# Kernel optimization log

Measured on AMD Instinct MI355X. Metric: run time of the kernel, lower is better.

## Reference

```python
import jax, jax.numpy as jnp
import numpy as np

N = 50000   # nodes
E = 640000  # edges
D_IN = 128
D_OUT = 128
EPS = 1e-5


def _layer_norm(x, gamma, beta):
    mu = jnp.mean(x, axis=-1, keepdims=True)
    var = jnp.mean(jnp.square(x - mu), axis=-1, keepdims=True)
    return (x - mu) * jax.lax.rsqrt(var + EPS) * gamma + beta


def _sage_conv(x, src, dst, w_l, b_l, w_r):
    # PyG SAGEConv (aggr='mean', root_weight=True, normalize=False):
    #   out = lin_l(mean_{j in N(i)} x_j) + lin_r(x_i)
    msgs = x[src]                                             # [E, D]
    agg = jax.ops.segment_sum(msgs, dst, num_segments=N)      # [N, D]
    cnt = jax.ops.segment_sum(jnp.ones((E,), x.dtype), dst, num_segments=N)
    mean = agg / jnp.maximum(cnt, 1.0)[:, None]
    return mean @ w_l.T + b_l + x @ w_r.T


def setup_inputs() -> dict:
    key = jax.random.key(0)
    ks = jax.random.split(key, 12)
    s_in = 1.0 / np.sqrt(D_IN)
    s_out = 1.0 / np.sqrt(D_OUT)
    return {
        "x": jax.random.normal(ks[0], (N, D_IN), jnp.float32),
        "edges": jax.random.randint(ks[1], (2, E), 0, N),
        "dp_w": jax.random.uniform(ks[2], (D_OUT, D_IN), jnp.float32, -s_in, s_in),
        "dp_b": jnp.zeros((D_OUT,), jnp.float32),
        "sc_w": jax.random.uniform(ks[3], (D_OUT, D_IN), jnp.float32, -s_in, s_in),
        "sc_b": jnp.zeros((D_OUT,), jnp.float32),
        "g1_lw": jax.random.uniform(ks[4], (D_OUT, D_OUT), jnp.float32, -s_out, s_out),
        "g1_lb": jnp.zeros((D_OUT,), jnp.float32),
        "g1_rw": jax.random.uniform(ks[5], (D_OUT, D_OUT), jnp.float32, -s_out, s_out),
        "n1_g": jnp.ones((D_OUT,), jnp.float32),
        "n1_b": jnp.zeros((D_OUT,), jnp.float32),
        "g2_lw": jax.random.uniform(ks[6], (D_OUT, D_OUT), jnp.float32, -s_out, s_out),
        "g2_lb": jnp.zeros((D_OUT,), jnp.float32),
        "g2_rw": jax.random.uniform(ks[7], (D_OUT, D_OUT), jnp.float32, -s_out, s_out),
        "n2_g": jnp.ones((D_OUT,), jnp.float32),
        "n2_b": jnp.zeros((D_OUT,), jnp.float32),
    }


def reference(x, edges, dp_w, dp_b, sc_w, sc_b, g1_lw, g1_lb, g1_rw, n1_g, n1_b,
              g2_lw, g2_lb, g2_rw, n2_g, n2_b):
    gelu = lambda v: jax.nn.gelu(v, approximate=False)
    src, dst = edges[0], edges[1]
    shortcut = x @ sc_w.T + sc_b
    h = gelu(x @ dp_w.T + dp_b)
    h = _sage_conv(h, src, dst, g1_lw, g1_lb, g1_rw)
    h = gelu(_layer_norm(h, n1_g, n1_b))
    h = _sage_conv(h, src, dst, g2_lw, g2_lb, g2_rw)
    h = _layer_norm(h, n2_g, n2_b)
    return gelu(h + shortcut)
```

## Files before the change

### kernel.cpp

```cpp
#include <hip/hip_runtime.h>
#include <hip/hip_bf16.h>
#include <math.h>

#define D 128
#define WS 136
#define FS 132
#define PB 128

typedef __attribute__((ext_vector_type(8))) short bf16x8;
typedef __attribute__((ext_vector_type(4))) float f32x4;

__device__ __forceinline__ unsigned short f2bf(float f){
  return (unsigned short)((__float_as_uint(f) + 0x8000u) >> 16);
}
__device__ __forceinline__ float bf2f(unsigned short h){
  return __uint_as_float(((unsigned)h) << 16);
}
__device__ __forceinline__ float bf2f_lo(unsigned v){
  return __uint_as_float(v << 16);
}
__device__ __forceinline__ float bf2f_hi(unsigned v){
  return __uint_as_float(v & 0xFFFF0000u);
}
__device__ __forceinline__ float gelu_fast(float v){
  float u = v * v;
  float arg = v * (1.5957691216f + 0.0713548163f * u);
  arg = fminf(arg, 60.0f);
  float e = __expf(arg);
  return v * e * __builtin_amdgcn_rcpf(e + 1.0f);
}

__global__ __launch_bounds__(256) void k_prepcnt(const float* s0, const float* s1,
    const float* s2, const float* s3, const float* s4, const float* s5,
    unsigned short* dst, const int* __restrict__ edst, int* __restrict__ cnt,
    int E, int nbuck, int epb){
  __shared__ int hist[512];
  if (blockIdx.x < 48){
    int gt = blockIdx.x * 256 + threadIdx.x;
    int m = gt >> 11;
    int r = gt & 2047;
    int f = r >> 6, lane = r & 63;
    int t = f & 7, kk = f >> 3;
    int row = t * 16 + (lane & 15);
    int col = kk * 32 + (lane >> 4) * 8;
    const float* src;
    if (m == 0) src = s0; else if (m == 1) src = s1; else if (m == 2) src = s2;
    else if (m == 3) src = s3; else if (m == 4) src = s4; else src = s5;
    src += row * 128 + col;
    float4 a = *(const float4*)src;
    float4 bb = *(const float4*)(src + 4);
    bf16x8 o;
    o[0] = (short)f2bf(a.x);  o[1] = (short)f2bf(a.y);
    o[2] = (short)f2bf(a.z);  o[3] = (short)f2bf(a.w);
    o[4] = (short)f2bf(bb.x); o[5] = (short)f2bf(bb.y);
    o[6] = (short)f2bf(bb.z); o[7] = (short)f2bf(bb.w);
    int pair = m >> 1, half = m & 1;
    *(bf16x8*)(dst + (size_t)pair * 32768 + (((size_t)f * 2 + half) * 64 + lane) * 8) = o;
    return;
  }
  int blk = blockIdx.x - 48;
  for (int b = threadIdx.x; b < nbuck; b += 256) hist[b] = 0;
  __syncthreads();
  int start = blk * epb;
  int end = min(E, start + epb);
  for (int e = start + threadIdx.x; e < end; e += 256)
    atomicAdd(&hist[edst[e] >> 7], 1);
  __syncthreads();
  for (int b = threadIdx.x; b < nbuck; b += 256) cnt[blk * nbuck + b] = hist[b];
}

__global__ __launch_bounds__(128) void k_scanA(const int* __restrict__ cnt,
    int* __restrict__ offs_rel, int* __restrict__ tot, int nbuck){
  __shared__ int sm[128];
  int b = blockIdx.x, t = threadIdx.x;
  int v = cnt[t * nbuck + b];
  sm[t] = v; __syncthreads();
  for (int ofs = 1; ofs < 128; ofs <<= 1){
    int u = (t >= ofs) ? sm[t - ofs] : 0;
    __syncthreads();
    sm[t] += u;
    __syncthreads();
  }
  offs_rel[t * nbuck + b] = sm[t] - v;
  if (t == 127) tot[b] = sm[127];
}

__global__ __launch_bounds__(256) void k_pscatter(const int* __restrict__ esrc,
    const int* __restrict__ edst, const int* __restrict__ offs_rel,
    const int* __restrict__ tot, unsigned* __restrict__ ebuf,
    int E, int nbuck, int epb){
  __shared__ int stot[512];
  __shared__ int loff[512];
  for (int b = threadIdx.x; b < nbuck; b += 256) stot[b] = tot[b];
  __syncthreads();
  for (int b = threadIdx.x; b < nbuck; b += 256){
    int s = 0;
    for (int j = 0; j < b; j++) s += stot[j];
    loff[b] = s + offs_rel[blockIdx.x * nbuck + b];
  }
  __syncthreads();
  int start = blockIdx.x * epb;
  int end = min(E, start + epb);
  for (int e = start + threadIdx.x; e < end; e += 256){
    int s = esrc[e], d = edst[e];
    int b = d >> 7;
    int pos = atomicAdd(&loff[b], 1);
    ebuf[pos] = (unsigned)s | ((unsigned)(d & 127) << 16);
  }
}

__global__ __launch_bounds__(256) void k_csrin(
    const unsigned* __restrict__ ebuf, const int* __restrict__ tot,
    int* __restrict__ off, int* __restrict__ csr,
    const float* __restrict__ x, const unsigned short* __restrict__ wp,
    const float* __restrict__ scb, const float* __restrict__ dpb,
    unsigned short* __restrict__ sbuf, unsigned short* __restrict__ hbuf,
    int N, int E, int nbuck){
  __shared__ int cnt[128], pref[128], curs[128];
  __shared__ int stot[512], red[256];
  __shared__ unsigned short tile[64 * WS];
  int tid = threadIdx.x;
  if ((int)blockIdx.x < nbuck){
    int b = blockIdx.x;
    for (int j = tid; j < nbuck; j += 256) stot[j] = tot[j];
    __syncthreads();
    int part = 0;
    for (int j = tid; j < b; j += 256) part += stot[j];
    red[tid] = part;
    __syncthreads();
    for (int ofs = 128; ofs > 0; ofs >>= 1){
      if (tid < ofs) red[tid] += red[tid + ofs];
      __syncthreads();
    }
    int start = red[0];
    int end = start + stot[b];
    if (tid < 128) cnt[tid] = 0;
    __syncthreads();
    for (int e = start + tid; e < end; e += 256)
      atomicAdd(&cnt[ebuf[e] >> 16], 1);
    __syncthreads();
    if (tid < 128) pref[tid] = cnt[tid];
    __syncthreads();
    for (int ofs = 1; ofs < 128; ofs <<= 1){
      int v = 0;
      if (tid < 128 && tid >= ofs) v = pref[tid - ofs];
      __syncthreads();
      if (tid < 128) pref[tid] += v;
      __syncthreads();
    }
    if (tid < 128){
      int ex = pref[tid] - cnt[tid];
      curs[tid] = ex;
      int node = b * 128 + tid;
      if (node < N) off[node] = start + ex;
    }
    if (b == 0 && tid == 0) off[N] = E;
    __syncthreads();
    for (int e = start + tid; e < end; e += 256){
      unsigned u = ebuf[e];
      int d = u >> 16;
      int p = atomicAdd(&curs[d], 1);
      csr[start + p] = (int)(u & 0xFFFFu);
    }
    return;
  }
  int bx = blockIdx.x - nbuck;
  int w = tid >> 6, lane = tid & 63, quad = lane >> 4, l16 = lane & 15;
  int nbb = bx * 64;
  int nb = nbb + w * 16;
  int arow = min(nb + l16, N - 1);
  f32x4 acc[2][8];
  #pragma unroll
  for (int m = 0; m < 2; m++)
    #pragma unroll
    for (int t = 0; t < 8; t++) acc[m][t] = (f32x4){0.f, 0.f, 0.f, 0.f};
  #pragma unroll
  for (int kk = 0; kk < 4; kk++){
    const float* xp = x + (size_t)arow * D + kk * 32 + quad * 8;
    float4 xa = *(const float4*)xp;
    float4 xb = *(const float4*)(xp + 4);
    bf16x8 a;
    a[0] = (short)f2bf(xa.x); a[1] = (short)f2bf(xa.y);
    a[2] = (short)f2bf(xa.z); a[3] = (short)f2bf(xa.w);
    a[4] = (short)f2bf(xb.x); a[5] = (short)f2bf(xb.y);
    a[6] = (short)f2bf(xb.z); a[7] = (short)f2bf(xb.w);
    #pragma unroll
    for (int t = 0; t < 8; t++){
      size_t fo = (((size_t)(kk * 8 + t) * 2) * 64 + lane) * 8;
      bf16x8 b0 = *(const bf16x8*)(wp + fo);
      bf16x8 b1 = *(const bf16x8*)(wp + fo + 512);
      acc[0][t] = __builtin_amdgcn_mfma_f32_16x16x32_bf16(a, b0, acc[0][t], 0, 0, 0);
      acc[1][t] = __builtin_amdgcn_mfma_f32_16x16x32_bf16(a, b1, acc[1][t], 0, 0, 0);
    }
  }
  #pragma unroll
  for (int m = 0; m < 2; m++){
    const float* bias = m ? dpb : scb;
    #pragma unroll
    for (int t = 0; t < 8; t++){
      float bv = bias[t * 16 + l16];
      #pragma unroll
      for (int r = 0; r < 4; r++){
        int nl = w * 16 + quad * 4 + r;
        float v = acc[m][t][r] + bv;
        if (m) v = gelu_fast(v);
        tile[nl * WS + t * 16 + l16] = f2bf(v);
      }
    }
    __syncthreads();
    unsigned short* dst = m ? hbuf : sbuf;
    #pragma unroll
    for (int i = 0; i < 4; i++){
      int c = tid + 256 * i;
      int nl = c >> 4, j = c & 15;
      int node = nbb + nl;
      if (node < N)
        *(bf16x8*)(dst + (size_t)node * D + j * 8) = *(const bf16x8*)(tile + nl * WS + j * 8);
    }
    __syncthreads();
  }
}

__global__ __launch_bounds__(256) void k_gather(
    const unsigned short* __restrict__ hin,
    const int* __restrict__ off, const int* __restrict__ csr,
    unsigned short* __restrict__ mout, int N){
  int tid = threadIdx.x;
  int node = blockIdx.x * 16 + (tid >> 4);
  int l16 = tid & 15;
  if (node >= N) return;
  int s0 = off[node], s1 = off[node + 1];
  float acc[8];
  #pragma unroll
  for (int c = 0; c < 8; c++) acc[c] = 0.f;
  if (s1 > s0){
    const unsigned short* hp = hin + l16 * 8;
    int nn[8];
    #pragma unroll
    for (int i = 0; i < 8; i++) nn[i] = csr[min(s0 + i, s1 - 1)];
    for (int e = s0; e < s1; e += 8){
      uint4 v[8];
      #pragma unroll
      for (int i = 0; i < 8; i++)
        v[i] = *(const uint4*)(hp + (size_t)nn[i] * D);
      #pragma unroll
      for (int i = 0; i < 8; i++) nn[i] = csr[min(e + 8 + i, s1 - 1)];
      #pragma unroll
      for (int i = 0; i < 8; i++){
        float m = (e + i < s1) ? 1.f : 0.f;
        acc[0] += m * bf2f_lo(v[i].x);
        acc[1] += m * bf2f_hi(v[i].x);
        acc[2] += m * bf2f_lo(v[i].y);
        acc[3] += m * bf2f_hi(v[i].y);
        acc[4] += m * bf2f_lo(v[i].z);
        acc[5] += m * bf2f_hi(v[i].z);
        acc[6] += m * bf2f_lo(v[i].w);
        acc[7] += m * bf2f_hi(v[i].w);
      }
    }
  }
  float inv = 1.f / (float)max(s1 - s0, 1);
  bf16x8 o;
  #pragma unroll
  for (int c = 0; c < 8; c++) o[c] = (short)f2bf(acc[c] * inv);
  *(bf16x8*)(mout + (size_t)node * D + l16 * 8) = o;
}

__global__ __launch_bounds__(256) void k_gemm(
    const unsigned short* __restrict__ hin,
    const unsigned short* __restrict__ mbuf,
    const unsigned short* __restrict__ wp,
    const float* __restrict__ lb, const float* __restrict__ gamma,
    const float* __restrict__ beta,
    const unsigned short* __restrict__ sbuf,
    unsigned short* __restrict__ hout, float* __restrict__ fout, int N, int mode){
  extern __shared__ char smraw[];
  unsigned short* stile = (unsigned short*)smraw;
  float* ftile = (float*)smraw;
  int tid = threadIdx.x;
  int nbb = blockIdx.x * 64;
  int w = tid >> 6, lane = tid & 63, quad = lane >> 4, l16 = lane & 15;
  int nb = nbb + w * 16;
  int arow = min(nb + l16, N - 1);
  bf16x8 am[4], ah[4];
  #pragma unroll
  for (int kk = 0; kk < 4; kk++){
    am[kk] = *(const bf16x8*)(mbuf + (size_t)arow * D + kk * 32 + quad * 8);
    ah[kk] = *(const bf16x8*)(hin + (size_t)arow * D + kk * 32 + quad * 8);
  }
  f32x4 acc[8];
  #pragma unroll
  for (int t = 0; t < 8; t++) acc[t] = (f32x4){0.f, 0.f, 0.f, 0.f};
  #pragma unroll
  for (int kk = 0; kk < 4; kk++){
    #pragma unroll
    for (int t = 0; t < 8; t++){
      size_t fo = (((size_t)(kk * 8 + t) * 2) * 64 + lane) * 8;
      bf16x8 bl = *(const bf16x8*)(wp + fo);
      bf16x8 br = *(const bf16x8*)(wp + fo + 512);
      acc[t] = __builtin_amdgcn_mfma_f32_16x16x32_bf16(am[kk], bl, acc[t], 0, 0, 0);
      acc[t] = __builtin_amdgcn_mfma_f32_16x16x32_bf16(ah[kk], br, acc[t], 0, 0, 0);
    }
  }
  float lbv[8], gv[8], bv[8];
  #pragma unroll
  for (int t = 0; t < 8; t++){
    lbv[t] = lb[t * 16 + l16];
    gv[t] = gamma[t * 16 + l16];
    bv[t] = beta[t * 16 + l16];
  }
  float mu[4], rs[4];
  #pragma unroll
  for (int r = 0; r < 4; r++){
    float s = 0.f, qq = 0.f;
    #pragma unroll
    for (int t = 0; t < 8; t++){
      float v = acc[t][r] + lbv[t];
      acc[t][r] = v;
      s += v; qq += v * v;
    }
    s += __shfl_xor(s, 1); qq += __shfl_xor(qq, 1);
    s += __shfl_xor(s, 2); qq += __shfl_xor(qq, 2);
    s += __shfl_xor(s, 4); qq += __shfl_xor(qq, 4);
    s += __shfl_xor(s, 8); qq += __shfl_xor(qq, 8);
    float m_ = s * (1.f / 128.f);
    mu[r] = m_;
    rs[r] = rsqrtf(qq * (1.f / 128.f) - m_ * m_ + 1e-5f);
  }
  if (mode == 0){
    #pragma unroll
    for (int t = 0; t < 8; t++)
      #pragma unroll
      for (int r = 0; r < 4; r++){
        int nl = w * 16 + quad * 4 + r;
        float v = (acc[t][r] - mu[r]) * rs[r] * gv[t] + bv[t];
        stile[nl * WS + t * 16 + l16] = f2bf(gelu_fast(v));
      }
    __syncthreads();
    #pragma unroll
    for (int i = 0; i < 4; i++){
      int c = tid + 256 * i;
      int nl = c >> 4, j = c & 15;
      int node = nbb + nl;
      if (node < N)
        *(bf16x8*)(hout + (size_t)node * D + j * 8) = *(const bf16x8*)(stile + nl * WS + j * 8);
    }
  } else {
    #pragma unroll
    for (int i = 0; i < 4; i++){
      int c = tid + 256 * i;
      int nl = c >> 4, j = c & 15;
      int node = nbb + nl;
      bf16x8 v = (bf16x8){0,0,0,0,0,0,0,0};
      if (node < N) v = *(const bf16x8*)(sbuf + (size_t)node * D + j * 8);
      *(bf16x8*)(stile + nl * WS + j * 8) = v;
    }
    __syncthreads();
    float sc[8][4];
    #pragma unroll
    for (int t = 0; t < 8; t++)
      #pragma unroll
      for (int r = 0; r < 4; r++){
        int nl = w * 16 + quad * 4 + r;
        sc[t][r] = bf2f(stile[nl * WS + t * 16 + l16]);
      }
    __syncthreads();
    #pragma unroll
    for (int t = 0; t < 8; t++)
      #pragma unroll
      for (int r = 0; r < 4; r++){
        int nl = w * 16 + quad * 4 + r;
        float v = (acc[t][r] - mu[r]) * rs[r] * gv[t] + bv[t];
        ftile[nl * FS + t * 16 + l16] = gelu_fast(v + sc[t][r]);
      }
    __syncthreads();
    #pragma unroll
    for (int i = 0; i < 8; i++){
      int c = tid + 256 * i;
      int nl = c >> 5, j = c & 31;
      int node = nbb + nl;
      if (node < N)
        *(float4*)(fout + (size_t)node * D + j * 4) = *(const float4*)(ftile + nl * FS + j * 4);
    }
  }
}

extern "C" void kernel_launch(void* const* d_in, const int* in_sizes, int n_in,
                              void* d_out, int out_size, void* d_ws, size_t ws_size,
                              hipStream_t stream){
  const float* x     = (const float*)d_in[0];
  const int*   edges = (const int*)d_in[1];
  const float* dp_w  = (const float*)d_in[2];
  const float* dp_b  = (const float*)d_in[3];
  const float* sc_w  = (const float*)d_in[4];
  const float* sc_b  = (const float*)d_in[5];
  const float* g1_lw = (const float*)d_in[6];
  const float* g1_lb = (const float*)d_in[7];
  const float* g1_rw = (const float*)d_in[8];
  const float* n1_g  = (const float*)d_in[9];
  const float* n1_b  = (const float*)d_in[10];
  const float* g2_lw = (const float*)d_in[11];
  const float* g2_lb = (const float*)d_in[12];
  const float* g2_rw = (const float*)d_in[13];
  const float* n2_g  = (const float*)d_in[14];
  const float* n2_b  = (const float*)d_in[15];

  const int N = in_sizes[0] / D;
  const int E = in_sizes[1] / 2;
  const int* esrc = edges;
  const int* edst = edges + E;
  const int nbuck = (N + 127) >> 7;
  const int epb = (E + PB - 1) / PB;

  char* base = (char*)d_ws;
  size_t cur = 0;
  auto carve = [&](size_t b) -> char* {
    char* p = base + cur;
    cur = (cur + b + 255) & ~(size_t)255;
    return p;
  };
  unsigned* ebuf  = (unsigned*)carve((size_t)E * 4);
  int* cnt        = (int*)carve((size_t)PB * nbuck * 4);
  int* offs_rel   = (int*)carve((size_t)PB * nbuck * 4);
  int* tot        = (int*)carve((size_t)nbuck * 4);
  int* off        = (int*)carve((size_t)(N + 1) * 4);
  int* csr        = (int*)carve((size_t)E * 4);
  unsigned short* wb    = (unsigned short*)carve((size_t)3 * 32768 * 2);
  unsigned short* hbuf  = (unsigned short*)carve((size_t)N * D * 2);
  unsigned short* h1buf = (unsigned short*)carve((size_t)N * D * 2);
  unsigned short* sbuf  = (unsigned short*)carve((size_t)N * D * 2);
  unsigned short* mbuf  = (unsigned short*)carve((size_t)N * D * 2);

  unsigned short* wp0 = wb;
  unsigned short* wp1 = wb + 32768;
  unsigned short* wp2 = wb + 2 * 32768;

  float* out = (float*)d_out;

  k_prepcnt<<<48 + PB, 256, 0, stream>>>(sc_w, dp_w, g1_lw, g1_rw, g2_lw, g2_rw,
                                         wb, edst, cnt, E, nbuck, epb);
  k_scanA<<<nbuck, 128, 0, stream>>>(cnt, offs_rel, tot, nbuck);
  k_pscatter<<<PB, 256, 0, stream>>>(esrc, edst, offs_rel, tot, ebuf, E, nbuck, epb);

  const int nin = (N + 63) / 64;
  k_csrin<<<nbuck + nin, 256, 0, stream>>>(ebuf, tot, off, csr,
                                           x, wp0, sc_b, dp_b, sbuf, hbuf,
                                           N, E, nbuck);

  const int ngat = (N + 15) / 16;
  k_gather<<<ngat, 256, 0, stream>>>(hbuf, off, csr, mbuf, N);
  k_gemm<<<nin, 256, 17408, stream>>>(hbuf, mbuf, wp1, g1_lb, n1_g, n1_b,
                                      nullptr, h1buf, nullptr, N, 0);
  k_gather<<<ngat, 256, 0, stream>>>(h1buf, off, csr, mbuf, N);
  k_gemm<<<nin, 256, 33792, stream>>>(h1buf, mbuf, wp2, g2_lb, n2_g, n2_b,
                                      sbuf, nullptr, out, N, 1);
}
```

Baseline: 238.3 us.

## Simplify CSR build with global atomics and fuse mean-gather into layer GEMM

The bucketed multi-pass CSR construction (histogram, scan, partition scatter, per-bucket sort) is replaced by a per-node global-atomic count, a single-block 1024-thread scan, and an atomic scatter fill. The neighbor mean aggregation is moved into the GEMM kernel, which writes it to a shared-memory tile instead of a global buffer. This removes kernel launches and the global round trip of the aggregated features. The trade-offs are a serial single-block scan, heavy global atomic contention, a CSR order that is no longer deterministic, and fewer blocks doing the gather inside the GEMM kernel.

```diff
diff --git a/kernel.cpp b/kernel.cpp
--- a/kernel.cpp
+++ b/kernel.cpp
@@ -5,7 +5,8 @@
 #define D 128
 #define WS 136
 #define FS 132
-#define PB 128
+#define CB 128
+#define FB 256
 
 typedef __attribute__((ext_vector_type(8))) short bf16x8;
 typedef __attribute__((ext_vector_type(4))) float f32x4;
@@ -30,11 +31,10 @@
   return v * e * __builtin_amdgcn_rcpf(e + 1.0f);
 }
 
-__global__ __launch_bounds__(256) void k_prepcnt(const float* s0, const float* s1,
+__global__ __launch_bounds__(256) void k_prep(const float* s0, const float* s1,
     const float* s2, const float* s3, const float* s4, const float* s5,
     unsigned short* dst, const int* __restrict__ edst, int* __restrict__ cnt,
-    int E, int nbuck, int epb){
-  __shared__ int hist[512];
+    int E, int epb){
   if (blockIdx.x < 48){
     int gt = blockIdx.x * 256 + threadIdx.x;
     int m = gt >> 11;
@@ -59,112 +59,57 @@
     return;
   }
   int blk = blockIdx.x - 48;
-  for (int b = threadIdx.x; b < nbuck; b += 256) hist[b] = 0;
-  __syncthreads();
   int start = blk * epb;
   int end = min(E, start + epb);
   for (int e = start + threadIdx.x; e < end; e += 256)
-    atomicAdd(&hist[edst[e] >> 7], 1);
+    atomicAdd(&cnt[edst[e]], 1);
+}
+
+__global__ __launch_bounds__(1024) void k_scan(const int* __restrict__ cnt,
+    int* __restrict__ off, int* __restrict__ cur, int N, int E){
+  __shared__ int ps[1024];
+  int t = threadIdx.x;
+  int C = (N + 1023) >> 10;
+  int b0 = t * C, b1 = min(N, b0 + C);
+  int s = 0;
+  for (int i = b0; i < b1; i++) s += cnt[i];
+  ps[t] = s;
   __syncthreads();
-  for (int b = threadIdx.x; b < nbuck; b += 256) cnt[blk * nbuck + b] = hist[b];
-}
-
-__global__ __launch_bounds__(128) void k_scanA(const int* __restrict__ cnt,
-    int* __restrict__ offs_rel, int* __restrict__ tot, int nbuck){
-  __shared__ int sm[128];
-  int b = blockIdx.x, t = threadIdx.x;
-  int v = cnt[t * nbuck + b];
-  sm[t] = v; __syncthreads();
-  for (int ofs = 1; ofs < 128; ofs <<= 1){
-    int u = (t >= ofs) ? sm[t - ofs] : 0;
-    __syncthreads();
-    sm[t] += u;
-    __syncthreads();
-  }
-  offs_rel[t * nbuck + b] = sm[t] - v;
-  if (t == 127) tot[b] = sm[127];
-}
-
-__global__ __launch_bounds__(256) void k_pscatter(const int* __restrict__ esrc,
-    const int* __restrict__ edst, const int* __restrict__ offs_rel,
-    const int* __restrict__ tot, unsigned* __restrict__ ebuf,
-    int E, int nbuck, int epb){
-  __shared__ int stot[512];
-  __shared__ int loff[512];
-  for (int b = threadIdx.x; b < nbuck; b += 256) stot[b] = tot[b];
-  __syncthreads();
-  for (int b = threadIdx.x; b < nbuck; b += 256){
-    int s = 0;
-    for (int j = 0; j < b; j++) s += stot[j];
-    loff[b] = s + offs_rel[blockIdx.x * nbuck + b];
-  }
-  __syncthreads();
-  int start = blockIdx.x * epb;
-  int end = min(E, start + epb);
-  for (int e = start + threadIdx.x; e < end; e += 256){
-    int s = esrc[e], d = edst[e];
-    int b = d >> 7;
-    int pos = atomicAdd(&loff[b], 1);
-    ebuf[pos] = (unsigned)s | ((unsigned)(d & 127) << 16);
-  }
-}
-
-__global__ __launch_bounds__(256) void k_csrin(
-    const unsigned* __restrict__ ebuf, const int* __restrict__ tot,
-    int* __restrict__ off, int* __restrict__ csr,
+  for (int ofs = 1; ofs < 1024; ofs <<= 1){
+    int u = (t >= ofs) ? ps[t - ofs] : 0;
+    __syncthreads();
+    ps[t] += u;
+    __syncthreads();
+  }
+  int run = ps[t] - s;
+  for (int i = b0; i < b1; i++){
+    off[i] = run;
+    cur[i] = run;
+    run += cnt[i];
+  }
+  if (t == 1023) off[N] = E;
+}
+
+__global__ __launch_bounds__(256) void k_fillin(
+    const int* __restrict__ esrc, const int* __restrict__ edst,
+    int* __restrict__ cur, int* __restrict__ csr,
     const float* __restrict__ x, const unsigned short* __restrict__ wp,
     const float* __restrict__ scb, const float* __restrict__ dpb,
     unsigned short* __restrict__ sbuf, unsigned short* __restrict__ hbuf,
-    int N, int E, int nbuck){
-  __shared__ int cnt[128], pref[128], curs[128];
-  __shared__ int stot[512], red[256];
+    int N, int E, int epb){
   __shared__ unsigned short tile[64 * WS];
   int tid = threadIdx.x;
-  if ((int)blockIdx.x < nbuck){
-    int b = blockIdx.x;
-    for (int j = tid; j < nbuck; j += 256) stot[j] = tot[j];
-    __syncthreads();
-    int part = 0;
-    for (int j = tid; j < b; j += 256) part += stot[j];
-    red[tid] = part;
-    __syncthreads();
-    for (int ofs = 128; ofs > 0; ofs >>= 1){
-      if (tid < ofs) red[tid] += red[tid + ofs];
-      __syncthreads();
-    }
-    int start = red[0];
-    int end = start + stot[b];
-    if (tid < 128) cnt[tid] = 0;
-    __syncthreads();
-    for (int e = start + tid; e < end; e += 256)
-      atomicAdd(&cnt[ebuf[e] >> 16], 1);
-    __syncthreads();
-    if (tid < 128) pref[tid] = cnt[tid];
-    __syncthreads();
-    for (int ofs = 1; ofs < 128; ofs <<= 1){
-      int v = 0;
-      if (tid < 128 && tid >= ofs) v = pref[tid - ofs];
-      __syncthreads();
-      if (tid < 128) pref[tid] += v;
-      __syncthreads();
-    }
-    if (tid < 128){
-      int ex = pref[tid] - cnt[tid];
-      curs[tid] = ex;
-      int node = b * 128 + tid;
-      if (node < N) off[node] = start + ex;
-    }
-    if (b == 0 && tid == 0) off[N] = E;
-    __syncthreads();
+  if ((int)blockIdx.x < FB){
+    int start = blockIdx.x * epb;
+    int end = min(E, start + epb);
     for (int e = start + tid; e < end; e += 256){
-      unsigned u = ebuf[e];
-      int d = u >> 16;
-      int p = atomicAdd(&curs[d], 1);
-      csr[start + p] = (int)(u & 0xFFFFu);
+      int d = edst[e];
+      int p = atomicAdd(&cur[d], 1);
+      csr[p] = esrc[e];
     }
     return;
   }
-  int bx = blockIdx.x - nbuck;
+  int bx = blockIdx.x - FB;
   int w = tid >> 6, lane = tid & 63, quad = lane >> 4, l16 = lane & 15;
   int nbb = bx * 64;
   int nb = nbb + w * 16;
@@ -221,71 +166,72 @@
   }
 }
 
-__global__ __launch_bounds__(256) void k_gather(
+__global__ __launch_bounds__(256) void k_layer(
     const unsigned short* __restrict__ hin,
     const int* __restrict__ off, const int* __restrict__ csr,
-    unsigned short* __restrict__ mout, int N){
-  int tid = threadIdx.x;
-  int node = blockIdx.x * 16 + (tid >> 4);
-  int l16 = tid & 15;
-  if (node >= N) return;
-  int s0 = off[node], s1 = off[node + 1];
-  float acc[8];
-  #pragma unroll
-  for (int c = 0; c < 8; c++) acc[c] = 0.f;
-  if (s1 > s0){
-    const unsigned short* hp = hin + l16 * 8;
-    int nn[8];
-    #pragma unroll
-    for (int i = 0; i < 8; i++) nn[i] = csr[min(s0 + i, s1 - 1)];
-    for (int e = s0; e < s1; e += 8){
-      uint4 v[8];
-      #pragma unroll
-      for (int i = 0; i < 8; i++)
-        v[i] = *(const uint4*)(hp + (size_t)nn[i] * D);
-      #pragma unroll
-      for (int i = 0; i < 8; i++) nn[i] = csr[min(e + 8 + i, s1 - 1)];
-      #pragma unroll
-      for (int i = 0; i < 8; i++){
-        float m = (e + i < s1) ? 1.f : 0.f;
-        acc[0] += m * bf2f_lo(v[i].x);
-        acc[1] += m * bf2f_hi(v[i].x);
-        acc[2] += m * bf2f_lo(v[i].y);
-        acc[3] += m * bf2f_hi(v[i].y);
-        acc[4] += m * bf2f_lo(v[i].z);
-        acc[5] += m * bf2f_hi(v[i].z);
-        acc[6] += m * bf2f_lo(v[i].w);
-        acc[7] += m * bf2f_hi(v[i].w);
-      }
-    }
-  }
-  float inv = 1.f / (float)max(s1 - s0, 1);
-  bf16x8 o;
-  #pragma unroll
-  for (int c = 0; c < 8; c++) o[c] = (short)f2bf(acc[c] * inv);
-  *(bf16x8*)(mout + (size_t)node * D + l16 * 8) = o;
-}
-
-__global__ __launch_bounds__(256) void k_gemm(
-    const unsigned short* __restrict__ hin,
-    const unsigned short* __restrict__ mbuf,
     const unsigned short* __restrict__ wp,
     const float* __restrict__ lb, const float* __restrict__ gamma,
     const float* __restrict__ beta,
     const unsigned short* __restrict__ sbuf,
     unsigned short* __restrict__ hout, float* __restrict__ fout, int N, int mode){
   extern __shared__ char smraw[];
+  unsigned short* mtile = (unsigned short*)smraw;
   unsigned short* stile = (unsigned short*)smraw;
   float* ftile = (float*)smraw;
   int tid = threadIdx.x;
   int nbb = blockIdx.x * 64;
+  {
+    int g = tid >> 4, l16g = tid & 15;
+    const unsigned short* hp = hin + l16g * 8;
+    #pragma unroll
+    for (int pass = 0; pass < 4; pass++){
+      int nl = pass * 16 + g;
+      int nodec = min(nbb + nl, N - 1);
+      int s0 = off[nodec], s1 = off[nodec + 1];
+      float acc[8];
+      #pragma unroll
+      for (int c = 0; c < 8; c++) acc[c] = 0.f;
+      if (s1 > s0){
+        int nn[8];
+        #pragma unroll
+        for (int i = 0; i < 8; i++) nn[i] = csr[min(s0 + i, s1 - 1)];
+        for (int e = s0; e < s1; e += 8){
+          uint4 v[8];
+          #pragma unroll
+          for (int i = 0; i < 8; i++)
+            v[i] = *(const uint4*)(hp + (size_t)nn[i] * D);
+          #pragma unroll
+          for (int i = 0; i < 8; i++) nn[i] = csr[min(e + 8 + i, s1 - 1)];
+          #pragma unroll
+          for (int i = 0; i < 8; i++){
+            float m = (e + i < s1) ? 1.f : 0.f;
+            acc[0] += m * bf2f_lo(v[i].x);
+            acc[1] += m * bf2f_hi(v[i].x);
+            acc[2] += m * bf2f_lo(v[i].y);
+            acc[3] += m * bf2f_hi(v[i].y);
+            acc[4] += m * bf2f_lo(v[i].z);
+            acc[5] += m * bf2f_hi(v[i].z);
+            acc[6] += m * bf2f_lo(v[i].w);
+            acc[7] += m * bf2f_hi(v[i].w);
+          }
+        }
+      }
+      float inv = 1.f / (float)max(s1 - s0, 1);
+      bf16x8 o;
+      #pragma unroll
+      for (int c = 0; c < 8; c++) o[c] = (short)f2bf(acc[c] * inv);
+      *(bf16x8*)(mtile + nl * WS + l16g * 8) = o;
+    }
+  }
+  __syncthreads();
   int w = tid >> 6, lane = tid & 63, quad = lane >> 4, l16 = lane & 15;
   int nb = nbb + w * 16;
   int arow = min(nb + l16, N - 1);
+  int mrow = w * 16 + l16;
   bf16x8 am[4], ah[4];
   #pragma unroll
   for (int kk = 0; kk < 4; kk++){
-    am[kk] = *(const bf16x8*)(mbuf + (size_t)arow * D + kk * 32 + quad * 8);
+    am[kk] = *(const bf16x8*)(mtile + mrow * WS + kk * 32 + quad * 8);
     ah[kk] = *(const bf16x8*)(hin + (size_t)arow * D + kk * 32 + quad * 8);
   }
   f32x4 acc[8];
@@ -327,6 +273,7 @@
     mu[r] = m_;
     rs[r] = rsqrtf(qq * (1.f / 128.f) - m_ * m_ + 1e-5f);
   }
+  __syncthreads();
   if (mode == 0){
     #pragma unroll
     for (int t = 0; t < 8; t++)
@@ -409,27 +356,22 @@
   const int E = in_sizes[1] / 2;
   const int* esrc = edges;
   const int* edst = edges + E;
-  const int nbuck = (N + 127) >> 7;
-  const int epb = (E + PB - 1) / PB;
 
   char* base = (char*)d_ws;
-  size_t cur = 0;
+  size_t cur_ = 0;
   auto carve = [&](size_t b) -> char* {
-    char* p = base + cur;
-    cur = (cur + b + 255) & ~(size_t)255;
+    char* p = base + cur_;
+    cur_ = (cur_ + b + 255) & ~(size_t)255;
     return p;
   };
-  unsigned* ebuf  = (unsigned*)carve((size_t)E * 4);
-  int* cnt        = (int*)carve((size_t)PB * nbuck * 4);
-  int* offs_rel   = (int*)carve((size_t)PB * nbuck * 4);
-  int* tot        = (int*)carve((size_t)nbuck * 4);
+  int* cnt        = (int*)carve((size_t)N * 4);
+  int* curs       = (int*)carve((size_t)N * 4);
   int* off        = (int*)carve((size_t)(N + 1) * 4);
   int* csr        = (int*)carve((size_t)E * 4);
   unsigned short* wb    = (unsigned short*)carve((size_t)3 * 32768 * 2);
   unsigned short* hbuf  = (unsigned short*)carve((size_t)N * D * 2);
   unsigned short* h1buf = (unsigned short*)carve((size_t)N * D * 2);
   unsigned short* sbuf  = (unsigned short*)carve((size_t)N * D * 2);
-  unsigned short* mbuf  = (unsigned short*)carve((size_t)N * D * 2);
 
   unsigned short* wp0 = wb;
   unsigned short* wp1 = wb + 32768;
@@ -437,21 +379,19 @@
 
   float* out = (float*)d_out;
 
-  k_prepcnt<<<48 + PB, 256, 0, stream>>>(sc_w, dp_w, g1_lw, g1_rw, g2_lw, g2_rw,
-                                         wb, edst, cnt, E, nbuck, epb);
-  k_scanA<<<nbuck, 128, 0, stream>>>(cnt, offs_rel, tot, nbuck);
-  k_pscatter<<<PB, 256, 0, stream>>>(esrc, edst, offs_rel, tot, ebuf, E, nbuck, epb);
-
+  const int epb_c = (E + CB - 1) / CB;
+  const int epb_f = (E + FB - 1) / FB;
   const int nin = (N + 63) / 64;
-  k_csrin<<<nbuck + nin, 256, 0, stream>>>(ebuf, tot, off, csr,
-                                           x, wp0, sc_b, dp_b, sbuf, hbuf,
-                                           N, E, nbuck);
-
-  const int ngat = (N + 15) / 16;
-  k_gather<<<ngat, 256, 0, stream>>>(hbuf, off, csr, mbuf, N);
-  k_gemm<<<nin, 256, 17408, stream>>>(hbuf, mbuf, wp1, g1_lb, n1_g, n1_b,
-                                      nullptr, h1buf, nullptr, N, 0);
-  k_gather<<<ngat, 256, 0, stream>>>(h1buf, off, csr, mbuf, N);
-  k_gemm<<<nin, 256, 33792, stream>>>(h1buf, mbuf, wp2, g2_lb, n2_g, n2_b,
-                                      sbuf, nullptr, out, N, 1);
-}
+
+  hipMemsetAsync(cnt, 0, (size_t)N * 4, stream);
+  k_prep<<<48 + CB, 256, 0, stream>>>(sc_w, dp_w, g1_lw, g1_rw, g2_lw, g2_rw,
+                                      wb, edst, cnt, E, epb_c);
+  k_scan<<<1, 1024, 0, stream>>>(cnt, off, curs, N, E);
+  k_fillin<<<FB + nin, 256, 0, stream>>>(esrc, edst, curs, csr,
+                                         x, wp0, sc_b, dp_b, sbuf, hbuf,
+                                         N, E, epb_f);
+  k_layer<<<nin, 256, 17408, stream>>>(hbuf, off, csr, wp1, g1_lb, n1_g, n1_b,
+                                       nullptr, h1buf, nullptr, N, 0);
+  k_layer<<<nin, 256, 33792, stream>>>(h1buf, off, csr, wp2, g2_lb, n2_g, n2_b,
+                                       sbuf, nullptr, out, N, 1);
+}
```

Measured after the change: 362.8 us. 1.52x slower.

## Fuse neighbor mean-aggregation into SAGE GEMM kernel via shared-memory tile

Applied to the files above, without the earlier changes.

Merges the separate gather (mean aggregation) kernel into the per-layer GEMM kernel. Each 64-node block now aggregates its own neighbor means into a shared-memory tile and feeds the MFMA A operand from LDS instead of a global mean buffer. This removes the global write and reread of the N×128 mean buffer and one launch per layer. In exchange, each block runs four serial gather passes of 16 nodes before its GEMM, with fewer blocks in flight to hide gather latency, and needs an extra barrier before the shared tile is reused for output staging.

```diff
diff --git a/kernel.cpp b/kernel.cpp
--- a/kernel.cpp
+++ b/kernel.cpp
@@ -221,71 +221,72 @@
   }
 }
 
-__global__ __launch_bounds__(256) void k_gather(
+__global__ __launch_bounds__(256) void k_layer(
     const unsigned short* __restrict__ hin,
     const int* __restrict__ off, const int* __restrict__ csr,
-    unsigned short* __restrict__ mout, int N){
-  int tid = threadIdx.x;
-  int node = blockIdx.x * 16 + (tid >> 4);
-  int l16 = tid & 15;
-  if (node >= N) return;
-  int s0 = off[node], s1 = off[node + 1];
-  float acc[8];
-  #pragma unroll
-  for (int c = 0; c < 8; c++) acc[c] = 0.f;
-  if (s1 > s0){
-    const unsigned short* hp = hin + l16 * 8;
-    int nn[8];
-    #pragma unroll
-    for (int i = 0; i < 8; i++) nn[i] = csr[min(s0 + i, s1 - 1)];
-    for (int e = s0; e < s1; e += 8){
-      uint4 v[8];
-      #pragma unroll
-      for (int i = 0; i < 8; i++)
-        v[i] = *(const uint4*)(hp + (size_t)nn[i] * D);
-      #pragma unroll
-      for (int i = 0; i < 8; i++) nn[i] = csr[min(e + 8 + i, s1 - 1)];
-      #pragma unroll
-      for (int i = 0; i < 8; i++){
-        float m = (e + i < s1) ? 1.f : 0.f;
-        acc[0] += m * bf2f_lo(v[i].x);
-        acc[1] += m * bf2f_hi(v[i].x);
-        acc[2] += m * bf2f_lo(v[i].y);
-        acc[3] += m * bf2f_hi(v[i].y);
-        acc[4] += m * bf2f_lo(v[i].z);
-        acc[5] += m * bf2f_hi(v[i].z);
-        acc[6] += m * bf2f_lo(v[i].w);
-        acc[7] += m * bf2f_hi(v[i].w);
-      }
-    }
-  }
-  float inv = 1.f / (float)max(s1 - s0, 1);
-  bf16x8 o;
-  #pragma unroll
-  for (int c = 0; c < 8; c++) o[c] = (short)f2bf(acc[c] * inv);
-  *(bf16x8*)(mout + (size_t)node * D + l16 * 8) = o;
-}
-
-__global__ __launch_bounds__(256) void k_gemm(
-    const unsigned short* __restrict__ hin,
-    const unsigned short* __restrict__ mbuf,
     const unsigned short* __restrict__ wp,
     const float* __restrict__ lb, const float* __restrict__ gamma,
     const float* __restrict__ beta,
     const unsigned short* __restrict__ sbuf,
     unsigned short* __restrict__ hout, float* __restrict__ fout, int N, int mode){
   extern __shared__ char smraw[];
+  unsigned short* mtile = (unsigned short*)smraw;
   unsigned short* stile = (unsigned short*)smraw;
   float* ftile = (float*)smraw;
   int tid = threadIdx.x;
   int nbb = blockIdx.x * 64;
+  {
+    int g = tid >> 4, l16g = tid & 15;
+    const unsigned short* hp = hin + l16g * 8;
+    #pragma unroll
+    for (int pass = 0; pass < 4; pass++){
+      int nl = pass * 16 + g;
+      int nodec = min(nbb + nl, N - 1);
+      int s0 = off[nodec], s1 = off[nodec + 1];
+      float acc[8];
+      #pragma unroll
+      for (int c = 0; c < 8; c++) acc[c] = 0.f;
+      if (s1 > s0){
+        int nn[8];
+        #pragma unroll
+        for (int i = 0; i < 8; i++) nn[i] = csr[min(s0 + i, s1 - 1)];
+        for (int e = s0; e < s1; e += 8){
+          uint4 v[8];
+          #pragma unroll
+          for (int i = 0; i < 8; i++)
+            v[i] = *(const uint4*)(hp + (size_t)nn[i] * D);
+          #pragma unroll
+          for (int i = 0; i < 8; i++) nn[i] = csr[min(e + 8 + i, s1 - 1)];
+          #pragma unroll
+          for (int i = 0; i < 8; i++){
+            float m = (e + i < s1) ? 1.f : 0.f;
+            acc[0] += m * bf2f_lo(v[i].x);
+            acc[1] += m * bf2f_hi(v[i].x);
+            acc[2] += m * bf2f_lo(v[i].y);
+            acc[3] += m * bf2f_hi(v[i].y);
+            acc[4] += m * bf2f_lo(v[i].z);
+            acc[5] += m * bf2f_hi(v[i].z);
+            acc[6] += m * bf2f_lo(v[i].w);
+            acc[7] += m * bf2f_hi(v[i].w);
+          }
+        }
+      }
+      float inv = 1.f / (float)max(s1 - s0, 1);
+      bf16x8 o;
+      #pragma unroll
+      for (int c = 0; c < 8; c++) o[c] = (short)f2bf(acc[c] * inv);
+      *(bf16x8*)(mtile + nl * WS + l16g * 8) = o;
+    }
+  }
+  __syncthreads();
   int w = tid >> 6, lane = tid & 63, quad = lane >> 4, l16 = lane & 15;
   int nb = nbb + w * 16;
   int arow = min(nb + l16, N - 1);
+  int mrow = w * 16 + l16;
   bf16x8 am[4], ah[4];
   #pragma unroll
   for (int kk = 0; kk < 4; kk++){
-    am[kk] = *(const bf16x8*)(mbuf + (size_t)arow * D + kk * 32 + quad * 8);
+    am[kk] = *(const bf16x8*)(mtile + mrow * WS + kk * 32 + quad * 8);
     ah[kk] = *(const bf16x8*)(hin + (size_t)arow * D + kk * 32 + quad * 8);
   }
   f32x4 acc[8];
@@ -327,6 +328,7 @@
     mu[r] = m_;
     rs[r] = rsqrtf(qq * (1.f / 128.f) - m_ * m_ + 1e-5f);
   }
+  __syncthreads();
   if (mode == 0){
     #pragma unroll
     for (int t = 0; t < 8; t++)
@@ -429,7 +431,6 @@
   unsigned short* hbuf  = (unsigned short*)carve((size_t)N * D * 2);
   unsigned short* h1buf = (unsigned short*)carve((size_t)N * D * 2);
   unsigned short* sbuf  = (unsigned short*)carve((size_t)N * D * 2);
-  unsigned short* mbuf  = (unsigned short*)carve((size_t)N * D * 2);
 
   unsigned short* wp0 = wb;
   unsigned short* wp1 = wb + 32768;
@@ -447,11 +448,8 @@
                                            x, wp0, sc_b, dp_b, sbuf, hbuf,
                                            N, E, nbuck);
 
-  const int ngat = (N + 15) / 16;
-  k_gather<<<ngat, 256, 0, stream>>>(hbuf, off, csr, mbuf, N);
-  k_gemm<<<nin, 256, 17408, stream>>>(hbuf, mbuf, wp1, g1_lb, n1_g, n1_b,
-                                      nullptr, h1buf, nullptr, N, 0);
-  k_gather<<<ngat, 256, 0, stream>>>(h1buf, off, csr, mbuf, N);
-  k_gemm<<<nin, 256, 33792, stream>>>(h1buf, mbuf, wp2, g2_lb, n2_g, n2_b,
-                                      sbuf, nullptr, out, N, 1);
-}
+  k_layer<<<nin, 256, 17408, stream>>>(hbuf, off, csr, wp1, g1_lb, n1_g, n1_b,
+                                       nullptr, h1buf, nullptr, N, 0);
+  k_layer<<<nin, 256, 33792, stream>>>(h1buf, off, csr, wp2, g2_lb, n2_g, n2_b,
+                                       sbuf, nullptr, out, N, 1);
+}
```

Result: faster. 233.0 us (-2.2%).
